# Performance work log

Hardware: AMD Instinct MI355X
Metric: run time of the kernel (lower is better)

The kernel has to match this reference:

```python
import jax, jax.numpy as jnp
import numpy as np

B, N, D, H = 8, 1024, 768, 12
HD = D // H
SCALE = HD ** -0.5

def setup_inputs() -> dict:
    key = jax.random.key(0)
    k1, k2, k3, k4 = jax.random.split(key, 4)
    x = jax.random.normal(k1, (B, N, D), dtype=jnp.float32)
    weight = jax.random.uniform(k2, (B, N), dtype=jnp.float32)
    W_qkv = jax.random.normal(k3, (D, 3 * D), dtype=jnp.float32) * (D ** -0.5)
    W_msa = jax.random.normal(k4, (D, D), dtype=jnp.float32) * (D ** -0.5)
    b_msa = jnp.zeros((D,), dtype=jnp.float32)
    return {"x": x, "weight": weight, "W_qkv": W_qkv, "W_msa": W_msa, "b_msa": b_msa}

def reference(x, weight, W_qkv, W_msa, b_msa):
    # QKV projection (no bias), then elementwise per-token gate
    qkv = jnp.einsum('bnd,de->bne', x, W_qkv)          # [B,N,3D]
    qkv = weight[:, :, None] * qkv
    qkv = qkv.reshape(B, N, 3, H, HD).transpose(2, 0, 3, 1, 4)  # [3,B,H,N,hd]
    q, k, v = qkv[0], qkv[1], qkv[2]
    A = jnp.einsum('bhnd,bhmd->bhnm', q, k) * SCALE    # [B,H,N,N]
    A = jax.nn.softmax(A, axis=-1)
    out = jnp.einsum('bhnm,bhmd->bhnd', A, v)          # [B,H,N,hd]
    out = out.transpose(0, 2, 1, 3).reshape(B, N, D)
    return jnp.einsum('bnd,de->bne', out, W_msa) + b_msa
```

## Files before the change

### kernel.cpp

```cpp
#include <hip/hip_runtime.h>
#include <hip/hip_bf16.h>


typedef __attribute__((ext_vector_type(8))) short bf8;
typedef __attribute__((ext_vector_type(4))) float f4;
typedef __attribute__((ext_vector_type(2))) unsigned u32x2;

#define QSCALE 0.1803368801111204f

static __device__ __forceinline__ short bf16_of(float f) {
    union { float f; unsigned u; } a; a.f = f;
    unsigned r = a.u + 0x7FFFu + ((a.u >> 16) & 1u);
    return (short)(r >> 16);
}

static __device__ __forceinline__ unsigned bfpk(float lo, float hi) {
    float2 t; t.x = lo; t.y = hi;
    __hip_bfloat162 b = __float22bfloat162_rn(t);
    union { __hip_bfloat162 b; unsigned u; } c; c.b = b;
    return c.u;
}

static __device__ __forceinline__ void async16(const short* g, short* l) {
    __builtin_amdgcn_global_load_lds(
        (const __attribute__((address_space(1))) void*)g,
        (__attribute__((address_space(3))) void*)l, 16, 0, 0);
}

__global__ __launch_bounds__(256) void k_cvt(const float* __restrict__ src,
                                             const float* __restrict__ gate,
                                             short* __restrict__ dst, int n8) {
    int i = blockIdx.x * 256 + threadIdx.x;
    if (i >= n8) return;
    const float g = gate[i / 96];
    const f4* sp = (const f4*)src;
    f4 a = sp[2 * i], b = sp[2 * i + 1];
    union { bf8 v; short h[8]; } o;
    o.h[0] = bf16_of(a[0] * g); o.h[1] = bf16_of(a[1] * g);
    o.h[2] = bf16_of(a[2] * g); o.h[3] = bf16_of(a[3] * g);
    o.h[4] = bf16_of(b[0] * g); o.h[5] = bf16_of(b[1] * g);
    o.h[6] = bf16_of(b[2] * g); o.h[7] = bf16_of(b[3] * g);
    ((bf8*)dst)[i] = o.v;
}

__global__ __launch_bounds__(256) void k_transpose(const float* __restrict__ w,
                                                   short* __restrict__ wt,
                                                   int K, int E) {
    __shared__ short t[64][65];
    const int k0 = blockIdx.y * 64, e0 = blockIdx.x * 64;
    const int tid = threadIdx.x;
#pragma unroll
    for (int p = 0; p < 16; ++p) {
        int idx = p * 256 + tid;
        int r = idx >> 6, c = idx & 63;
        t[r][c] = bf16_of(w[(k0 + r) * E + e0 + c]);
    }
    __syncthreads();
#pragma unroll
    for (int p = 0; p < 16; ++p) {
        int idx = p * 256 + tid;
        int r = idx >> 6, c = idx & 63;
        wt[(e0 + r) * K + k0 + c] = t[c][r];
    }
}

static __device__ __forceinline__ void gemm128(const short* __restrict__ gA,
                                               const short* __restrict__ gB,
                                               short* As, short* Bs,
                                               f4 acc[4][4]) {
    const int tid = threadIdx.x, lane = tid & 63;
    const int l16 = lane & 15, quad = lane >> 4, rx = l16 & 7;
    const int wm = (tid >> 6) & 1, wn = tid >> 7;

    for (int k0 = 0; k0 < 768; k0 += 64) {
#pragma unroll
        for (int c = 0; c < 4; ++c) {
            int p = c * 256 + tid;
            int row = p >> 3, slot = p & 7;
            int gc = slot ^ (row & 7);
            async16(gA + row * 768 + k0 + gc * 8, As + p * 8);
            async16(gB + row * 768 + k0 + gc * 8, Bs + p * 8);
        }
        __syncthreads();
#pragma unroll
        for (int ks = 0; ks < 2; ++ks) {
            bf8 af[4], bfr[4];
#pragma unroll
            for (int mt = 0; mt < 4; ++mt)
                af[mt] = *(const bf8*)(As + (wm * 64 + mt * 16 + l16) * 64 +
                                       (((ks * 4 + quad) ^ rx) * 8));
#pragma unroll
            for (int nt = 0; nt < 4; ++nt)
                bfr[nt] = *(const bf8*)(Bs + (wn * 64 + nt * 16 + l16) * 64 +
                                        (((ks * 4 + quad) ^ rx) * 8));
#pragma unroll
            for (int mt = 0; mt < 4; ++mt)
#pragma unroll
                for (int nt = 0; nt < 4; ++nt)
                    acc[mt][nt] = __builtin_amdgcn_mfma_f32_16x16x32_bf16(
                        af[mt], bfr[nt], acc[mt][nt], 0, 0, 0);
        }
        __syncthreads();
    }
}

__global__ __launch_bounds__(256) void k_gemm_qkv(
        const short* __restrict__ xb, const short* __restrict__ wtq,
        short* __restrict__ qb, short* __restrict__ kb, short* __restrict__ vt) {
    __shared__ short smem[16896];
    short* As = smem;
    short* Bs = smem + 8192;
    const int tid = threadIdx.x, lane = tid & 63;
    const int l16 = lane & 15, quad = lane >> 4;
    const int wm = (tid >> 6) & 1, wn = tid >> 7;
    const int m0 = blockIdx.y * 128, n0 = blockIdx.x * 128;
    f4 z = {0.f, 0.f, 0.f, 0.f};
    f4 acc[4][4] = {{z,z,z,z},{z,z,z,z},{z,z,z,z},{z,z,z,z}};
    gemm128(xb + m0 * 768, wtq + n0 * 768, As, Bs, acc);

    const int which = n0 / 768;
    if (which < 2) {
#pragma unroll
        for (int mt = 0; mt < 4; ++mt) {
#pragma unroll
            for (int r = 0; r < 4; ++r) {
                const int row = m0 + wm * 64 + mt * 16 + quad * 4 + r;
                const int b = row >> 10, nn = row & 1023;
#pragma unroll
                for (int nt = 0; nt < 4; ++nt) {
                    const int ct = n0 + wn * 64 + nt * 16;
                    const int h = (ct - which * 768) >> 6;
                    const int hh = b * 12 + h;
                    const int hd = (ct & 63) + l16;
                    const float val = acc[mt][nt][r];
                    if (which == 0)
                        qb[(hh * 1024 + nn) * 64 + hd] = bf16_of(val * QSCALE);
                    else
                        kb[(hh * 1024 + nn) * 64 + hd] = bf16_of(val);
                }
            }
        }
    } else {
#pragma unroll
        for (int mt = 0; mt < 4; ++mt) {
#pragma unroll
            for (int r = 0; r < 4; ++r) {
                const int tok = wm * 64 + mt * 16 + quad * 4 + r;
#pragma unroll
                for (int nt = 0; nt < 4; ++nt) {
                    const int dim = wn * 64 + nt * 16 + l16;
                    smem[dim * 132 + tok] = bf16_of(acc[mt][nt][r]);
                }
            }
        }
        __syncthreads();
        const int b = m0 >> 10, nn0 = m0 & 1023;
#pragma unroll
        for (int ps = 0; ps < 8; ++ps) {
            const int row = ps * 16 + (tid >> 4);
            const int chunk = tid & 15;
            const int dg = (n0 - 1536) + row;
            const int h = dg >> 6, hd = dg & 63;
            bf8 val = *(const bf8*)(smem + row * 132 + chunk * 8);
            *(bf8*)(vt + ((b * 12 + h) * 64 + hd) * 1024 + nn0 + chunk * 8) = val;
        }
    }
}

__global__ __launch_bounds__(256) void k_gemm_final(
        const short* __restrict__ attn, const short* __restrict__ wtm,
        const float* __restrict__ bias, float* __restrict__ out) {
    __shared__ short smem[16384];
    short* As = smem;
    short* Bs = smem + 8192;
    const int lane = threadIdx.x & 63;
    const int l16 = lane & 15, quad = lane >> 4;
    const int wm = (threadIdx.x >> 6) & 1, wn = threadIdx.x >> 7;
    const int m0 = blockIdx.y * 128, n0 = blockIdx.x * 128;
    f4 z = {0.f, 0.f, 0.f, 0.f};
    f4 acc[4][4] = {{z,z,z,z},{z,z,z,z},{z,z,z,z},{z,z,z,z}};
    gemm128(attn + m0 * 768, wtm + n0 * 768, As, Bs, acc);
#pragma unroll
    for (int mt = 0; mt < 4; ++mt) {
#pragma unroll
        for (int r = 0; r < 4; ++r) {
            const int row = m0 + wm * 64 + mt * 16 + quad * 4 + r;
#pragma unroll
            for (int nt = 0; nt < 4; ++nt) {
                const int e = n0 + wn * 64 + nt * 16 + l16;
                out[row * 768 + e] = acc[mt][nt][r] + bias[e];
            }
        }
    }
}

__global__ __launch_bounds__(256) void k_attn(const short* __restrict__ qb,
                                              const short* __restrict__ kb,
                                              const short* __restrict__ vt,
                                              short* __restrict__ attn) {
    __shared__ short Ks[2][4096];
    __shared__ short Vs[2][4096];
    __shared__ unsigned Ps[4][16][20];
    const int tid = threadIdx.x, wave = tid >> 6, lane = tid & 63;
    const int l16 = lane & 15, quad = lane >> 4, rx = l16 & 7;
    const int bh = blockIdx.x;
    const int b = bh / 12, h = bh - b * 12;
    const int m_base = blockIdx.y * 128 + wave * 32;
    const short* qh = qb + bh * 65536;
    const short* kh = kb + bh * 65536;
    const short* vh = vt + bh * 65536;
    unsigned* pw = &Ps[wave][0][0];

    bf8 qf[2][2];
#pragma unroll
    for (int t = 0; t < 2; ++t) {
        const short* qp = qh + (m_base + t * 16 + l16) * 64 + quad * 8;
        qf[t][0] = *(const bf8*)(qp);
        qf[t][1] = *(const bf8*)(qp + 32);
    }
    union { bf8 v; short h[8]; } onef;
#pragma unroll
    for (int i = 0; i < 8; ++i) onef.h[i] = (short)0x3F80;

    f4 z = {0.f, 0.f, 0.f, 0.f};
    f4 acc[2][4] = {{z, z, z, z}, {z, z, z, z}};
    f4 accl[2] = {z, z};

    auto stage = [&](int buf, int j0) {
#pragma unroll
        for (int c = 0; c < 2; ++c) {
            int idx = c * 256 + tid;
            int row = idx >> 3;
            int sc = ((idx & 7) ^ (row & 7)) * 8;
            async16(kh + (j0 + row) * 64 + sc, Ks[buf] + idx * 8);
            async16(vh + row * 1024 + j0 + sc, Vs[buf] + idx * 8);
        }
    };

    stage(0, 0);
    int cur = 0;
    for (int it = 0; it < 16; ++it) {
        __syncthreads();
        if (it + 1 < 16) stage(cur ^ 1, (it + 1) * 64);
        const short* Kc = Ks[cur];
        const short* Vc = Vs[cur];

#pragma unroll
        for (int jj = 0; jj < 64; jj += 32) {
            const short* kr0 = Kc + (jj + l16) * 64;
            const short* kr1 = Kc + (jj + 16 + l16) * 64;
            bf8 k0a = *(const bf8*)(kr0 + ((quad ^ rx) * 8));
            bf8 k0b = *(const bf8*)(kr0 + (((4 | quad) ^ rx) * 8));
            bf8 k1a = *(const bf8*)(kr1 + ((quad ^ rx) * 8));
            bf8 k1b = *(const bf8*)(kr1 + (((4 | quad) ^ rx) * 8));

            bf8 pf[2];
#pragma unroll
            for (int t = 0; t < 2; ++t) {
                f4 s0 = z, s1 = z;
                s0 = __builtin_amdgcn_mfma_f32_16x16x32_bf16(k0a, qf[t][0], s0, 0, 0, 0);
                s0 = __builtin_amdgcn_mfma_f32_16x16x32_bf16(k0b, qf[t][1], s0, 0, 0, 0);
                s1 = __builtin_amdgcn_mfma_f32_16x16x32_bf16(k1a, qf[t][0], s1, 0, 0, 0);
                s1 = __builtin_amdgcn_mfma_f32_16x16x32_bf16(k1b, qf[t][1], s1, 0, 0, 0);
                float p0 = exp2f(s0[0]), p1 = exp2f(s0[1]);
                float p2 = exp2f(s0[2]), p3 = exp2f(s0[3]);
                float p4 = exp2f(s1[0]), p5 = exp2f(s1[1]);
                float p6 = exp2f(s1[2]), p7 = exp2f(s1[3]);
                u32x2 wa, wb;
                wa[0] = bfpk(p0, p1); wa[1] = bfpk(p2, p3);
                wb[0] = bfpk(p4, p5); wb[1] = bfpk(p6, p7);
                *(u32x2*)(pw + l16 * 20 + quad * 2) = wa;
                *(u32x2*)(pw + l16 * 20 + 8 + quad * 2) = wb;
                pf[t] = *(const bf8*)(pw + l16 * 20 + quad * 4);
                accl[t] = __builtin_amdgcn_mfma_f32_16x16x32_bf16(
                    onef.v, pf[t], accl[t], 0, 0, 0);
            }

#pragma unroll
            for (int dt = 0; dt < 4; ++dt) {
                int vrow = dt * 16 + l16;
                bf8 vf = *(const bf8*)(Vc + vrow * 64 +
                                       ((((jj >> 3) + quad) ^ rx) * 8));
                acc[0][dt] = __builtin_amdgcn_mfma_f32_16x16x32_bf16(vf, pf[0], acc[0][dt], 0, 0, 0);
                acc[1][dt] = __builtin_amdgcn_mfma_f32_16x16x32_bf16(vf, pf[1], acc[1][dt], 0, 0, 0);
            }
        }
        cur ^= 1;
    }

#pragma unroll
    for (int t = 0; t < 2; ++t) {
        const float inv = 1.f / accl[t][0];
        const int row = (b << 10) + m_base + t * 16 + l16;
        short* op = attn + row * 768 + h * 64 + quad * 4;
#pragma unroll
        for (int dt = 0; dt < 4; ++dt)
#pragma unroll
            for (int r = 0; r < 4; ++r)
                op[dt * 16 + r] = bf16_of(acc[t][dt][r] * inv);
    }
}

extern "C" void kernel_launch(void* const* d_in, const int* in_sizes, int n_in,
                              void* d_out, int out_size, void* d_ws, size_t ws_size,
                              hipStream_t stream) {
    const float* x    = (const float*)d_in[0];
    const float* gate = (const float*)d_in[1];
    const float* Wqkv = (const float*)d_in[2];
    const float* Wmsa = (const float*)d_in[3];
    const float* bmsa = (const float*)d_in[4];
    float* out = (float*)d_out;

    char* ws = (char*)d_ws;
    short* xb  = (short*)(ws);
    short* wtq = (short*)(ws + 12582912);
    short* wtm = (short*)(ws + 16121856);
    short* qb  = (short*)(ws + 17301504);
    short* kb  = (short*)(ws + 29884416);
    short* vt  = (short*)(ws + 42467328);
    short* attn = xb;

    k_cvt<<<3072, 256, 0, stream>>>(x, gate, xb, 786432);
    k_transpose<<<dim3(36, 12), 256, 0, stream>>>(Wqkv, wtq, 768, 2304);
    k_transpose<<<dim3(12, 12), 256, 0, stream>>>(Wmsa, wtm, 768, 768);
    k_gemm_qkv<<<dim3(18, 64), 256, 0, stream>>>(xb, wtq, qb, kb, vt);
    k_attn<<<dim3(96, 8), 256, 0, stream>>>(qb, kb, vt, attn);
    k_gemm_final<<<dim3(6, 64), 256, 0, stream>>>(attn, wtm, bmsa, out);
}
```

Measured before the change: 213.9 us.

## Keep P in registers via permuted K row mapping, dropping LDS round-trip

The attention kernel now loads K rows in a permuted order, so the score MFMA output lanes line up with the B-operand layout needed by the PV MFMA. The exponentiated probabilities can then be packed straight into the bf8 fragment without a per-wave LDS write and read. The LDS swizzle for K and V is changed to match the new access pattern, exp2f is swapped for the hardware exp2 builtin, and explicit waitcnt calls are added before the barriers. The permutation must be matched exactly between K and V or the results will be wrong.

```diff
diff --git a/kernel.cpp b/kernel.cpp
--- a/kernel.cpp
+++ b/kernel.cpp
@@ -4,7 +4,6 @@
 
 typedef __attribute__((ext_vector_type(8))) short bf8;
 typedef __attribute__((ext_vector_type(4))) float f4;
-typedef __attribute__((ext_vector_type(2))) unsigned u32x2;
 
 #define QSCALE 0.1803368801111204f
 
@@ -81,6 +80,7 @@
             async16(gA + row * 768 + k0 + gc * 8, As + p * 8);
             async16(gB + row * 768 + k0 + gc * 8, Bs + p * 8);
         }
+        __builtin_amdgcn_s_waitcnt(0);
         __syncthreads();
 #pragma unroll
         for (int ks = 0; ks < 2; ++ks) {
@@ -200,16 +200,23 @@
                                               short* __restrict__ attn) {
     __shared__ short Ks[2][4096];
     __shared__ short Vs[2][4096];
-    __shared__ unsigned Ps[4][16][20];
     const int tid = threadIdx.x, wave = tid >> 6, lane = tid & 63;
-    const int l16 = lane & 15, quad = lane >> 4, rx = l16 & 7;
+    const int l16 = lane & 15, quad = lane >> 4;
     const int bh = blockIdx.x;
     const int b = bh / 12, h = bh - b * 12;
     const int m_base = blockIdx.y * 128 + wave * 32;
     const short* qh = qb + bh * 65536;
     const short* kh = kb + bh * 65536;
     const short* vh = vt + bh * 65536;
-    unsigned* pw = &Ps[wave][0][0];
+
+    const int rA = ((l16 >> 2) << 3) + (l16 & 3);
+    const int fK = (((rA >> 3) & 1) << 2) + (rA & 3);
+    const int sK = (quad ^ fK) * 8;
+    const int oAlo = rA * 64 + sK;
+    const int oAhi = rA * 64 + (sK ^ 32);
+    const int oBlo = oAlo + 256, oBhi = oAhi + 256;
+    const int fV = (((l16 >> 3) & 1) << 2) + (l16 & 3);
+    const int oV = l16 * 64 + ((quad ^ fV) * 8);
 
     bf8 qf[2][2];
 #pragma unroll
@@ -231,15 +238,17 @@
         for (int c = 0; c < 2; ++c) {
             int idx = c * 256 + tid;
             int row = idx >> 3;
-            int sc = ((idx & 7) ^ (row & 7)) * 8;
-            async16(kh + (j0 + row) * 64 + sc, Ks[buf] + idx * 8);
-            async16(vh + row * 1024 + j0 + sc, Vs[buf] + idx * 8);
+            int fr = (((row >> 3) & 1) << 2) + (row & 3);
+            int gc = (idx & 7) ^ fr;
+            async16(kh + (j0 + row) * 64 + gc * 8, Ks[buf] + idx * 8);
+            async16(vh + row * 1024 + j0 + gc * 8, Vs[buf] + idx * 8);
         }
     };
 
     stage(0, 0);
     int cur = 0;
     for (int it = 0; it < 16; ++it) {
+        __builtin_amdgcn_s_waitcnt(0);
         __syncthreads();
         if (it + 1 < 16) stage(cur ^ 1, (it + 1) * 64);
         const short* Kc = Ks[cur];
@@ -247,40 +256,39 @@
 
 #pragma unroll
         for (int jj = 0; jj < 64; jj += 32) {
-            const short* kr0 = Kc + (jj + l16) * 64;
-            const short* kr1 = Kc + (jj + 16 + l16) * 64;
-            bf8 k0a = *(const bf8*)(kr0 + ((quad ^ rx) * 8));
-            bf8 k0b = *(const bf8*)(kr0 + (((4 | quad) ^ rx) * 8));
-            bf8 k1a = *(const bf8*)(kr1 + ((quad ^ rx) * 8));
-            bf8 k1b = *(const bf8*)(kr1 + (((4 | quad) ^ rx) * 8));
+            const short* kjj = Kc + jj * 64;
+            bf8 kAlo = *(const bf8*)(kjj + oAlo);
+            bf8 kAhi = *(const bf8*)(kjj + oAhi);
+            bf8 kBlo = *(const bf8*)(kjj + oBlo);
+            bf8 kBhi = *(const bf8*)(kjj + oBhi);
 
             bf8 pf[2];
 #pragma unroll
             for (int t = 0; t < 2; ++t) {
-                f4 s0 = z, s1 = z;
-                s0 = __builtin_amdgcn_mfma_f32_16x16x32_bf16(k0a, qf[t][0], s0, 0, 0, 0);
-                s0 = __builtin_amdgcn_mfma_f32_16x16x32_bf16(k0b, qf[t][1], s0, 0, 0, 0);
-                s1 = __builtin_amdgcn_mfma_f32_16x16x32_bf16(k1a, qf[t][0], s1, 0, 0, 0);
-                s1 = __builtin_amdgcn_mfma_f32_16x16x32_bf16(k1b, qf[t][1], s1, 0, 0, 0);
-                float p0 = exp2f(s0[0]), p1 = exp2f(s0[1]);
-                float p2 = exp2f(s0[2]), p3 = exp2f(s0[3]);
-                float p4 = exp2f(s1[0]), p5 = exp2f(s1[1]);
-                float p6 = exp2f(s1[2]), p7 = exp2f(s1[3]);
-                u32x2 wa, wb;
-                wa[0] = bfpk(p0, p1); wa[1] = bfpk(p2, p3);
-                wb[0] = bfpk(p4, p5); wb[1] = bfpk(p6, p7);
-                *(u32x2*)(pw + l16 * 20 + quad * 2) = wa;
-                *(u32x2*)(pw + l16 * 20 + 8 + quad * 2) = wb;
-                pf[t] = *(const bf8*)(pw + l16 * 20 + quad * 4);
+                f4 sA = z, sB = z;
+                sA = __builtin_amdgcn_mfma_f32_16x16x32_bf16(kAlo, qf[t][0], sA, 0, 0, 0);
+                sA = __builtin_amdgcn_mfma_f32_16x16x32_bf16(kAhi, qf[t][1], sA, 0, 0, 0);
+                sB = __builtin_amdgcn_mfma_f32_16x16x32_bf16(kBlo, qf[t][0], sB, 0, 0, 0);
+                sB = __builtin_amdgcn_mfma_f32_16x16x32_bf16(kBhi, qf[t][1], sB, 0, 0, 0);
+                float a0 = __builtin_amdgcn_exp2f(sA[0]);
+                float a1 = __builtin_amdgcn_exp2f(sA[1]);
+                float a2 = __builtin_amdgcn_exp2f(sA[2]);
+                float a3 = __builtin_amdgcn_exp2f(sA[3]);
+                float b0 = __builtin_amdgcn_exp2f(sB[0]);
+                float b1 = __builtin_amdgcn_exp2f(sB[1]);
+                float b2 = __builtin_amdgcn_exp2f(sB[2]);
+                float b3 = __builtin_amdgcn_exp2f(sB[3]);
+                union { bf8 v; unsigned u[4]; } p;
+                p.u[0] = bfpk(a0, a1); p.u[1] = bfpk(a2, a3);
+                p.u[2] = bfpk(b0, b1); p.u[3] = bfpk(b2, b3);
+                pf[t] = p.v;
                 accl[t] = __builtin_amdgcn_mfma_f32_16x16x32_bf16(
-                    onef.v, pf[t], accl[t], 0, 0, 0);
+                    onef.v, p.v, accl[t], 0, 0, 0);
             }
 
 #pragma unroll
             for (int dt = 0; dt < 4; ++dt) {
-                int vrow = dt * 16 + l16;
-                bf8 vf = *(const bf8*)(Vc + vrow * 64 +
-                                       ((((jj >> 3) + quad) ^ rx) * 8));
+                bf8 vf = *(const bf8*)(Vc + dt * 1024 + (oV ^ (jj ? 32 : 0)));
                 acc[0][dt] = __builtin_amdgcn_mfma_f32_16x16x32_bf16(vf, pf[0], acc[0][dt], 0, 0, 0);
                 acc[1][dt] = __builtin_amdgcn_mfma_f32_16x16x32_bf16(vf, pf[1], acc[1][dt], 0, 0, 0);
             }
```

After: 200.5 us. 6.2% less time.
